# Kernel optimization log

Measured on AMD Instinct MI355X. Metric: run time of the kernel, lower is better.

Reference implementation:

```python
import jax, jax.numpy as jnp
import numpy as np

B = 16384   # batch
S = 512     # state_size
A = 512     # action_size
H = 1024    # hidden_dim
L = 64      # latent_size
E = 6       # num_experts
G = 32      # gate hidden size
IN = S + L      # first-layer input size
INT = H + L     # intermediate input size
SIGMA = 0.05


def setup_inputs() -> dict:
    key = jax.random.key(0)
    ks = jax.random.split(key, 20)

    def u(k, shape, s):
        return jax.random.uniform(k, shape, jnp.float32, -s, s)

    inp = {}
    inp['state'] = jax.random.normal(ks[0], (B, S), jnp.float32)
    inp['latent'] = jax.random.normal(ks[1], (B, L), jnp.float32)
    # expert decoder layers: (E, J, K) weights, (E, K) biases; torch init: w ~ U(-3/sqrt(J), 3/sqrt(J)), b ~ U(-1/sqrt(J), 1/sqrt(J))
    dims = [(IN, H), (INT, H), (INT, H), (INT, A)]
    for i, (j, k_) in enumerate(dims):
        stdv = 1.0 / np.sqrt(j)
        inp[f'w{i}'] = u(ks[2 + 2 * i], (E, j, k_), 3.0 * stdv)
        inp[f'b{i}'] = u(ks[3 + 2 * i], (E, k_), stdv)
    # gating MLP: IN -> G -> G -> E
    gdims = [(IN, G), (G, G), (G, E)]
    for i, (a, b) in enumerate(gdims):
        s = 1.0 / np.sqrt(a)
        inp[f'gw{i}'] = u(ks[10 + 2 * i], (a, b), s)
        inp[f'gb{i}'] = u(ks[11 + 2 * i], (b,), s)
    return inp


def reference(state, latent, w0, b0, w1, b1, w2, b2, w3, b3,
              gw0, gb0, gw1, gb1, gw2, gb2):
    xc = jnp.concatenate([state, latent], axis=-1)          # [B, IN]
    # gating MLP with ELU activations, softmax over experts
    h = jax.nn.elu(xc @ gw0 + gb0)
    h = jax.nn.elu(h @ gw1 + gb1)
    coef = jax.nn.softmax(h @ gw2 + gb2, axis=-1)           # [B, E]

    layer_out = state
    ws = [w0, w1, w2, w3]
    bs = [b0, b1, b2, b3]
    for i in range(4):
        inp = jnp.concatenate([layer_out, latent], axis=-1)  # [B, J]
        # per-sample soft-mixed expert matmul + bias
        mixed = jnp.einsum('be,bj,ejk->bk', coef, inp, ws[i],
                           optimize=True) + coef @ bs[i]      # [B, K]
        layer_out = jax.nn.elu(mixed) if i < 3 else mixed

    # reparameterize with fixed sigma: mu + eps * sigma (eps from a fixed key for determinism)
    eps = jax.random.normal(jax.random.key(42), layer_out.shape, layer_out.dtype)
    return layer_out + eps * SIGMA
```

## Files before the change

kernel.cpp:

```cpp
#include <hip/hip_runtime.h>

typedef _Float16 f16;
typedef _Float16 half8 __attribute__((ext_vector_type(8)));
typedef float f32x4 __attribute__((ext_vector_type(4)));
typedef unsigned int u32;

#define B_    16384
#define E_    6
#define ASTR  1088
#define AOUT  512

__device__ __forceinline__ u32 swz(u32 row, u32 ch) {
  return row * 128u + ((ch ^ (row & 7u)) * 16u);
}

__device__ __forceinline__ float elu_f(float x) {
  return x > 0.f ? x : (__expf(x) - 1.f);
}

__device__ __forceinline__ half8 splat8(f16 s) {
  half8 v = {s, s, s, s, s, s, s, s};
  return v;
}

__device__ __forceinline__ void gload16(const f16* g, char* l) {
  __builtin_amdgcn_global_load_lds(
      (const __attribute__((address_space(1))) void*)g,
      (__attribute__((address_space(3))) void*)l, 16, 0, 0);
}

#define WAITVM(N) asm volatile("s_waitcnt vmcnt(" #N ")" ::: "memory")

__device__ __forceinline__ float jax_eps(u32 idx) {
  const u32 k0 = 0u, k1 = 42u;
  const u32 k2 = k0 ^ k1 ^ 0x1BD11BDAu;
  u32 x0 = 0u + k0, x1 = idx + k1;
#define TFR(r) { x0 += x1; x1 = (x1 << (r)) | (x1 >> (32 - (r))); x1 ^= x0; }
  TFR(13) TFR(15) TFR(26) TFR(6)   x0 += k1; x1 += k2 + 1u;
  TFR(17) TFR(29) TFR(16) TFR(24)  x0 += k2; x1 += k0 + 2u;
  TFR(13) TFR(15) TFR(26) TFR(6)   x0 += k0; x1 += k1 + 3u;
  TFR(17) TFR(29) TFR(16) TFR(24)  x0 += k1; x1 += k2 + 4u;
  TFR(13) TFR(15) TFR(26) TFR(6)   x0 += k2; x1 += k0 + 5u;
#undef TFR
  u32 bits = x0 ^ x1;
  float f = __uint_as_float(0x3f800000u | (bits >> 9)) - 1.0f;
  const float lo = -0.99999994f;
  float u = fmaxf(lo, fmaf(f, 2.0f, lo));
  float w = -__logf(fmaf(-u, u, 1.0f));
  float p;
  if (w < 5.0f) {
    w -= 2.5f;
    p = 2.81022636e-08f;
    p = fmaf(p, w, 3.43273939e-07f);
    p = fmaf(p, w, -3.5233877e-06f);
    p = fmaf(p, w, -4.39150654e-06f);
    p = fmaf(p, w, 0.00021858087f);
    p = fmaf(p, w, -0.00125372503f);
    p = fmaf(p, w, -0.00417768164f);
    p = fmaf(p, w, 0.246640727f);
    p = fmaf(p, w, 1.50140941f);
  } else {
    w = __fsqrt_rn(w) - 3.0f;
    p = -0.000200214257f;
    p = fmaf(p, w, 0.000100950558f);
    p = fmaf(p, w, 0.00134934322f);
    p = fmaf(p, w, -0.00367342844f);
    p = fmaf(p, w, 0.00573950773f);
    p = fmaf(p, w, -0.0076224613f);
    p = fmaf(p, w, 0.00943887047f);
    p = fmaf(p, w, 1.00167406f);
    p = fmaf(p, w, 2.83297682f);
  }
  return 1.41421356f * p * u;
}

__global__ void prep_act(const float* __restrict__ state, const float* __restrict__ latent,
                         f16* __restrict__ actA, f16* __restrict__ actB) {
  const u32 NS = (B_ * 512u) / 8u;
  const u32 NL = (B_ * 64u) / 8u;
  u32 i = blockIdx.x * 256u + threadIdx.x;
  if (i < NS) {
    u32 e = i * 8u;
    u32 b = e >> 9, c = e & 511u;
    float4 v0 = *(const float4*)(state + e);
    float4 v1 = *(const float4*)(state + e + 4);
    half8 h;
    h[0]=(f16)v0.x; h[1]=(f16)v0.y; h[2]=(f16)v0.z; h[3]=(f16)v0.w;
    h[4]=(f16)v1.x; h[5]=(f16)v1.y; h[6]=(f16)v1.z; h[7]=(f16)v1.w;
    *(half8*)(actA + (size_t)b * ASTR + c) = h;
  } else if (i < NS + NL) {
    u32 e = (i - NS) * 8u;
    u32 b = e >> 6, c = e & 63u;
    float4 v0 = *(const float4*)(latent + e);
    float4 v1 = *(const float4*)(latent + e + 4);
    half8 h;
    h[0]=(f16)v0.x; h[1]=(f16)v0.y; h[2]=(f16)v0.z; h[3]=(f16)v0.w;
    h[4]=(f16)v1.x; h[5]=(f16)v1.y; h[6]=(f16)v1.z; h[7]=(f16)v1.w;
    *(half8*)(actA + (size_t)b * ASTR + 512 + c) = h;
    *(half8*)(actA + (size_t)b * ASTR + 1024 + c) = h;
    *(half8*)(actB + (size_t)b * ASTR + 1024 + c) = h;
  }
}

__global__ void prep_gw0(const float* __restrict__ gw0, f16* __restrict__ g0hi,
                         f16* __restrict__ g0lo) {
  int i = blockIdx.x * 256 + threadIdx.x;
  if (i < 32 * 576) {
    int n = i / 576, j = i % 576;
    float v = gw0[j * 32 + n];
    f16 h = (f16)v;
    g0hi[i] = h;
    g0lo[i] = (f16)(v - (float)h);
  }
}

__global__ void transpose_w(const float* __restrict__ w, f16* __restrict__ wt,
                            int J, int K) {
  __shared__ float t[64][65];
  int tiles_j = J >> 6, tiles_k = K >> 6;
  int per_e = tiles_j * tiles_k;
  int bid = blockIdx.x;
  int e = bid / per_e, rem = bid % per_e;
  int jt = rem / tiles_k, kt = rem % tiles_k;
  int tid = threadIdx.x;
  int r = tid >> 2, c0 = (tid & 3) << 4;
  const float* src = w + ((size_t)e * J + (size_t)jt * 64 + r) * K + (size_t)kt * 64 + c0;
  float4 v0 = *(const float4*)(src);
  float4 v1 = *(const float4*)(src + 4);
  float4 v2 = *(const float4*)(src + 8);
  float4 v3 = *(const float4*)(src + 12);
  t[r][c0+0]=v0.x;  t[r][c0+1]=v0.y;  t[r][c0+2]=v0.z;  t[r][c0+3]=v0.w;
  t[r][c0+4]=v1.x;  t[r][c0+5]=v1.y;  t[r][c0+6]=v1.z;  t[r][c0+7]=v1.w;
  t[r][c0+8]=v2.x;  t[r][c0+9]=v2.y;  t[r][c0+10]=v2.z; t[r][c0+11]=v2.w;
  t[r][c0+12]=v3.x; t[r][c0+13]=v3.y; t[r][c0+14]=v3.z; t[r][c0+15]=v3.w;
  __syncthreads();
  int kr = tid >> 2, jq = (tid & 3) << 4;
  half8 p0, p1;
#pragma unroll
  for (int m = 0; m < 8; m++) {
    p0[m] = (f16)t[jq + m][kr];
    p1[m] = (f16)t[jq + 8 + m][kr];
  }
  f16* dst = wt + ((size_t)e * K + (size_t)kt * 64 + kr) * J + (size_t)jt * 64 + jq;
  *(half8*)(dst) = p0;
  *(half8*)(dst + 8) = p1;
}

__global__ __launch_bounds__(256) void gating_kernel(
    const float* __restrict__ state, const float* __restrict__ latent,
    const f16* __restrict__ g0hi, const f16* __restrict__ g0lo,
    const float* __restrict__ gb0, const float* __restrict__ gw1,
    const float* __restrict__ gb1, const float* __restrict__ gw2,
    const float* __restrict__ gb2, float* __restrict__ coefT) {
  __shared__ __align__(16) char sm[24576];
  __shared__ float h_lds[64][33];
  char* Ahi = sm;
  char* Alo = sm + 8192;
  char* Bhi = sm + 16384;
  char* Blo = sm + 20480;
  const int tid = threadIdx.x, lane = tid & 63, wave = tid >> 6;
  const int b0 = blockIdx.x * 64;

  f32x4 acc[2];
#pragma unroll
  for (int n = 0; n < 2; n++) {
    float v = gb0[n * 16 + (lane & 15)];
    f32x4 t = {v, v, v, v};
    acc[n] = t;
  }

  for (int kt = 0; kt < 9; ++kt) {
    __syncthreads();
    int r = tid >> 2, cq = (tid & 3) << 4;
    float xv[16];
    if (kt < 8) {
      const float* s = state + (size_t)(b0 + r) * 512 + kt * 64 + cq;
      *(float4*)(xv)      = *(const float4*)(s);
      *(float4*)(xv + 4)  = *(const float4*)(s + 4);
      *(float4*)(xv + 8)  = *(const float4*)(s + 8);
      *(float4*)(xv + 12) = *(const float4*)(s + 12);
    } else {
      const float* s = latent + (size_t)(b0 + r) * 64 + cq;
      *(float4*)(xv)      = *(const float4*)(s);
      *(float4*)(xv + 4)  = *(const float4*)(s + 4);
      *(float4*)(xv + 8)  = *(const float4*)(s + 8);
      *(float4*)(xv + 12) = *(const float4*)(s + 12);
    }
    half8 hh[2], hl[2];
#pragma unroll
    for (int q = 0; q < 2; q++)
#pragma unroll
      for (int i = 0; i < 8; i++) {
        float x = xv[q * 8 + i];
        f16 h = (f16)x;
        hh[q][i] = h;
        hl[q][i] = (f16)(x - (float)h);
      }
    *(half8*)(Ahi + swz(r, (tid & 3) * 2 + 0)) = hh[0];
    *(half8*)(Ahi + swz(r, (tid & 3) * 2 + 1)) = hh[1];
    *(half8*)(Alo + swz(r, (tid & 3) * 2 + 0)) = hl[0];
    *(half8*)(Alo + swz(r, (tid & 3) * 2 + 1)) = hl[1];
    int nb = tid >> 3, chb = tid & 7;
    half8 bh = *(const half8*)(g0hi + (size_t)nb * 576 + kt * 64 + chb * 8);
    half8 bl = *(const half8*)(g0lo + (size_t)nb * 576 + kt * 64 + chb * 8);
    *(half8*)(Bhi + swz(nb, chb)) = bh;
    *(half8*)(Blo + swz(nb, chb)) = bl;
    __syncthreads();
#pragma unroll
    for (int ks = 0; ks < 2; ks++) {
      int arow = wave * 16 + (lane & 15);
      int ch = ks * 4 + (lane >> 4);
      half8 ah = *(const half8*)(Ahi + swz(arow, ch));
      half8 al = *(const half8*)(Alo + swz(arow, ch));
#pragma unroll
      for (int n = 0; n < 2; n++) {
        int brow = n * 16 + (lane & 15);
        half8 wh = *(const half8*)(Bhi + swz(brow, ch));
        half8 wl = *(const half8*)(Blo + swz(brow, ch));
        acc[n] = __builtin_amdgcn_mfma_f32_16x16x32_f16(ah, wh, acc[n], 0, 0, 0);
        acc[n] = __builtin_amdgcn_mfma_f32_16x16x32_f16(al, wh, acc[n], 0, 0, 0);
        acc[n] = __builtin_amdgcn_mfma_f32_16x16x32_f16(ah, wl, acc[n], 0, 0, 0);
      }
    }
  }
#pragma unroll
  for (int n = 0; n < 2; n++)
#pragma unroll
    for (int i = 0; i < 4; i++) {
      int row = wave * 16 + (lane >> 4) * 4 + i;
      int col = n * 16 + (lane & 15);
      h_lds[row][col] = elu_f(acc[n][i]);
    }
  __syncthreads();
  {
    int row = tid & 63, q = tid >> 6;
    float a2[8];
#pragma unroll
    for (int o = 0; o < 8; o++) a2[o] = gb1[q * 8 + o];
    for (int j = 0; j < 32; j++) {
      float v = h_lds[row][j];
#pragma unroll
      for (int o = 0; o < 8; o++) a2[o] = fmaf(v, gw1[j * 32 + q * 8 + o], a2[o]);
    }
    __syncthreads();
#pragma unroll
    for (int o = 0; o < 8; o++) h_lds[row][q * 8 + o] = elu_f(a2[o]);
  }
  __syncthreads();
  if (wave == 0) {
    float lg[6];
#pragma unroll
    for (int e = 0; e < 6; e++) lg[e] = gb2[e];
    for (int j = 0; j < 32; j++) {
      float v = h_lds[lane][j];
#pragma unroll
      for (int e = 0; e < 6; e++) lg[e] = fmaf(v, gw2[j * 6 + e], lg[e]);
    }
    float mx = lg[0];
#pragma unroll
    for (int e = 1; e < 6; e++) mx = fmaxf(mx, lg[e]);
    float s = 0.f, pc[6];
#pragma unroll
    for (int e = 0; e < 6; e++) { pc[e] = __expf(lg[e] - mx); s += pc[e]; }
    float inv = 1.0f / s;
#pragma unroll
    for (int e = 0; e < 6; e++) coefT[e * B_ + b0 + lane] = pc[e] * inv;
  }
}

template <int J, int KOUT, int MODE>
__global__ __launch_bounds__(256, 3) void moe_gemm(
    const f16* __restrict__ act, const f16* __restrict__ wt,
    const float* __restrict__ coefT, const float* __restrict__ bias,
    f16* __restrict__ out_act, float* __restrict__ out_f32) {
  constexpr int NSUB = J / 64;
  constexpr int NTILE = KOUT / 64;
  __shared__ __align__(16) char sm[44032];
  float* const cfLds = (float*)(sm + 40960);

  const int tid = threadIdx.x;
  const int lane = tid & 63;
  const int wv = tid >> 6;
  const int wr = wv >> 1, wc = wv & 1;
  const int nwg = gridDim.x;
  const int cpx = nwg >> 3;
  const int bid = (blockIdx.x & 7) * cpx + (blockIdx.x >> 3);
  const int b0 = (bid / NTILE) * 128;
  const int n0 = (bid % NTILE) * 64;

  for (int i = tid; i < E_ * 128; i += 256) {
    int e = i >> 7, r = i & 127;
    cfLds[i] = coefT[e * B_ + b0 + r];
  }
  __syncthreads();

  f32x4 acc[4][2];
#pragma unroll
  for (int m = 0; m < 4; m++)
#pragma unroll
    for (int n = 0; n < 2; n++) {
      f32x4 z = {0.f, 0.f, 0.f, 0.f};
      acc[m][n] = z;
    }
#pragma unroll
  for (int e = 0; e < E_; e++) {
    float bv[2];
#pragma unroll
    for (int n = 0; n < 2; n++)
      bv[n] = bias[e * KOUT + n0 + wc * 32 + n * 16 + (lane & 15)];
#pragma unroll
    for (int m = 0; m < 4; m++)
#pragma unroll
      for (int i = 0; i < 4; i++) {
        float cv = cfLds[e * 128 + wr * 64 + m * 16 + (lane >> 4) * 4 + i];
#pragma unroll
        for (int n = 0; n < 2; n++) acc[m][n][i] = fmaf(cv, bv[n], acc[m][n][i]);
      }
  }

  u32 aVoff[4], bVoff[2];
#pragma unroll
  for (int i = 0; i < 4; i++) {
    int r = wv * 32 + i * 8 + (lane >> 3);
    aVoff[i] = (u32)(b0 + r) * ASTR + (u32)(((lane & 7) ^ (r & 7)) * 8);
  }
#pragma unroll
  for (int i = 0; i < 2; i++) {
    int r = wv * 16 + i * 8 + (lane >> 3);
    bVoff[i] = (u32)(n0 + r) * J + (u32)(((lane & 7) ^ (r & 7)) * 8);
  }

  char* const As = sm;

  auto stageA = [&](int ks) {
    const f16* ab = act + ks * 64;
#pragma unroll
    for (int i = 0; i < 4; i++)
      gload16(ab + aVoff[i], As + (wv * 4 + i) * 1024);
  };
  auto stageB = [&](int e, int ks, int buf) {
    const f16* wb = wt + (size_t)e * KOUT * J + ks * 64;
    char* Bs = sm + 16384 + buf * 8192;
#pragma unroll
    for (int i = 0; i < 2; i++)
      gload16(wb + bVoff[i], Bs + (wv * 2 + i) * 1024);
  };

  stageA(0);
  stageB(0, 0, 0);
  stageB(1, 0, 1);

  u32 aOff[2], bOff[2];
#pragma unroll
  for (int h = 0; h < 2; h++) {
    aOff[h] = swz(wr * 64 + (lane & 15), h * 4 + (lane >> 4));
    bOff[h] = swz(wc * 32 + (lane & 15), h * 4 + (lane >> 4));
  }
  const u32 cfOff = (u32)(wr * 64 + (lane & 15)) * 4u;

  half8 afr[2][4];

  auto compute = [&](int buf, int e, bool loadA) {
    char* Bcur = sm + 16384 + buf * 8192;
    if (loadA) {
#pragma unroll
      for (int h = 0; h < 2; h++)
#pragma unroll
        for (int m = 0; m < 4; m++)
          afr[h][m] = *(const half8*)(As + aOff[h] + m * 2048);
    }
    f16 cfh[4];
#pragma unroll
    for (int m = 0; m < 4; m++)
      cfh[m] = (f16)*(const float*)((const char*)cfLds + cfOff + e * 512 + m * 64);
#pragma unroll
    for (int h = 0; h < 2; h++) {
      half8 bf[2];
#pragma unroll
      for (int n = 0; n < 2; n++)
        bf[n] = *(const half8*)(Bcur + bOff[h] + n * 2048);
      __builtin_amdgcn_s_setprio(1);
#pragma unroll
      for (int m = 0; m < 4; m++) {
        half8 afs = afr[h][m] * splat8(cfh[m]);
#pragma unroll
        for (int n = 0; n < 2; n++)
          acc[m][n] = __builtin_amdgcn_mfma_f32_16x16x32_f16(afs, bf[n], acc[m][n], 0, 0, 0);
      }
      __builtin_amdgcn_s_setprio(0);
    }
  };

  for (int ks = 0; ks < NSUB - 1; ++ks) {
#pragma unroll
    for (int e = 0; e < 6; ++e) {
      if (e == 2 || e == 3) { WAITVM(6); } else { WAITVM(2); }
      __builtin_amdgcn_s_barrier();
      stageB((e + 2) % 6, ks + (e + 2) / 6, (e + 2) % 3);
      if (e == 1) stageA(ks + 1);
      compute(e % 3, e, e == 0);
    }
  }
  {
    const int ks = NSUB - 1;
#pragma unroll
    for (int e = 0; e < 6; ++e) {
      if (e == 5) { WAITVM(0); } else { WAITVM(2); }
      __builtin_amdgcn_s_barrier();
      if (e <= 3) stageB(e + 2, ks, (e + 2) % 3);
      compute(e % 3, e, e == 0);
    }
  }

#pragma unroll
  for (int m = 0; m < 4; m++)
#pragma unroll
    for (int n = 0; n < 2; n++)
#pragma unroll
      for (int i = 0; i < 4; i++) {
        int row = b0 + wr * 64 + m * 16 + (lane >> 4) * 4 + i;
        int col = n0 + wc * 32 + n * 16 + (lane & 15);
        float x = acc[m][n][i];
        if (MODE == 0) {
          out_act[(size_t)row * ASTR + col] = (f16)elu_f(x);
        } else {
          u32 idx = (u32)row * AOUT + col;
          out_f32[idx] = fmaf(0.05f, jax_eps(idx), x);
        }
      }
}

extern "C" void kernel_launch(void* const* d_in, const int* in_sizes, int n_in,
                              void* d_out, int out_size, void* d_ws, size_t ws_size,
                              hipStream_t stream) {
  (void)in_sizes; (void)n_in; (void)out_size; (void)ws_size;
  const float* state  = (const float*)d_in[0];
  const float* latent = (const float*)d_in[1];
  const float* w0 = (const float*)d_in[2];
  const float* b0 = (const float*)d_in[3];
  const float* w1 = (const float*)d_in[4];
  const float* b1 = (const float*)d_in[5];
  const float* w2 = (const float*)d_in[6];
  const float* b2 = (const float*)d_in[7];
  const float* w3 = (const float*)d_in[8];
  const float* b3 = (const float*)d_in[9];
  const float* gw0 = (const float*)d_in[10];
  const float* gb0 = (const float*)d_in[11];
  const float* gw1 = (const float*)d_in[12];
  const float* gb1 = (const float*)d_in[13];
  const float* gw2 = (const float*)d_in[14];
  const float* gb2 = (const float*)d_in[15];

  char* ws = (char*)d_ws;
  size_t off = 0;
  float* coefT = (float*)(ws + off); off += (size_t)E_ * B_ * 4;
  f16* actA = (f16*)(ws + off); off += (size_t)B_ * ASTR * 2;
  f16* actB = (f16*)(ws + off); off += (size_t)B_ * ASTR * 2;
  f16* wt0 = (f16*)(ws + off); off += (size_t)E_ * 1024 * 576 * 2;
  f16* wt1 = (f16*)(ws + off); off += (size_t)E_ * 1024 * 1088 * 2;
  f16* wt2 = (f16*)(ws + off); off += (size_t)E_ * 1024 * 1088 * 2;
  f16* wt3 = (f16*)(ws + off); off += (size_t)E_ * 512 * 1088 * 2;
  f16* g0hi = (f16*)(ws + off); off += 32 * 576 * 2;
  f16* g0lo = (f16*)(ws + off); off += 32 * 576 * 2;

  prep_act<<<4608, 256, 0, stream>>>(state, latent, actA, actB);
  prep_gw0<<<72, 256, 0, stream>>>(gw0, g0hi, g0lo);
  transpose_w<<<6 * 9 * 16, 256, 0, stream>>>(w0, wt0, 576, 1024);
  transpose_w<<<6 * 17 * 16, 256, 0, stream>>>(w1, wt1, 1088, 1024);
  transpose_w<<<6 * 17 * 16, 256, 0, stream>>>(w2, wt2, 1088, 1024);
  transpose_w<<<6 * 17 * 8, 256, 0, stream>>>(w3, wt3, 1088, 512);
  gating_kernel<<<256, 256, 0, stream>>>(state, latent, g0hi, g0lo, gb0, gw1, gb1,
                                         gw2, gb2, coefT);
  moe_gemm<576, 1024, 0><<<2048, 256, 0, stream>>>(actA, wt0, coefT, b0, actB, nullptr);
  moe_gemm<1088, 1024, 0><<<2048, 256, 0, stream>>>(actB, wt1, coefT, b1, actA, nullptr);
  moe_gemm<1088, 1024, 0><<<2048, 256, 0, stream>>>(actA, wt2, coefT, b2, actB, nullptr);
  moe_gemm<1088, 512, 1><<<1024, 256, 0, stream>>>(actB, wt3, coefT, b3, nullptr, (float*)d_out);
}
```

Measured before the change: 747.8 us.

## Software-pipeline LDS B-fragment reads into registers ahead of MFMA in MoE GEMM

Restructures the expert loop so the B-tile fragments for the next expert are read from LDS into a second register set while MFMAs for the current expert run (ping-pong bfA/bfB). It also prefetches three B stages up front and rewrites the loop as explicitly unrolled steps with lgkmcnt waits. Launch bounds are lowered from 3 to 2 waves-per-EU to give the compiler room for the extra fragment registers. The intent is to hide LDS read latency behind matrix math, at the cost of register pressure, possible lower occupancy, and more complex hand-scheduled synchronization.

```diff
diff --git a/kernel.cpp b/kernel.cpp
--- a/kernel.cpp
+++ b/kernel.cpp
@@ -30,6 +30,7 @@
 }
 
 #define WAITVM(N) asm volatile("s_waitcnt vmcnt(" #N ")" ::: "memory")
+#define LGKM0    asm volatile("s_waitcnt lgkmcnt(0)" ::: "memory")
 
 __device__ __forceinline__ float jax_eps(u32 idx) {
   const u32 k0 = 0u, k1 = 42u;
@@ -269,7 +270,7 @@
 }
 
 template <int J, int KOUT, int MODE>
-__global__ __launch_bounds__(256, 3) void moe_gemm(
+__global__ __launch_bounds__(256, 2) void moe_gemm(
     const f16* __restrict__ act, const f16* __restrict__ wt,
     const float* __restrict__ coefT, const float* __restrict__ bias,
     f16* __restrict__ out_act, float* __restrict__ out_f32) {
@@ -277,6 +278,10 @@
   constexpr int NTILE = KOUT / 64;
   __shared__ __align__(16) char sm[44032];
   float* const cfLds = (float*)(sm + 40960);
+  char* const As  = sm;
+  char* const B0s = sm + 16384;
+  char* const B1s = sm + 24576;
+  char* const B2s = sm + 32768;
 
   const int tid = threadIdx.x;
   const int lane = tid & 63;
@@ -330,86 +335,129 @@
     bVoff[i] = (u32)(n0 + r) * J + (u32)(((lane & 7) ^ (r & 7)) * 8);
   }
 
-  char* const As = sm;
-
   auto stageA = [&](int ks) {
     const f16* ab = act + ks * 64;
 #pragma unroll
     for (int i = 0; i < 4; i++)
       gload16(ab + aVoff[i], As + (wv * 4 + i) * 1024);
   };
-  auto stageB = [&](int e, int ks, int buf) {
+  auto stageB = [&](int e, int ks, char* Bs) {
     const f16* wb = wt + (size_t)e * KOUT * J + ks * 64;
-    char* Bs = sm + 16384 + buf * 8192;
 #pragma unroll
     for (int i = 0; i < 2; i++)
       gload16(wb + bVoff[i], Bs + (wv * 2 + i) * 1024);
   };
 
   stageA(0);
-  stageB(0, 0, 0);
-  stageB(1, 0, 1);
-
-  u32 aOff[2], bOff[2];
+  stageB(0, 0, B0s);
+  stageB(1, 0, B1s);
+  stageB(2, 0, B2s);
+
+  u32 aOffh[2], bOffh[2];
 #pragma unroll
   for (int h = 0; h < 2; h++) {
-    aOff[h] = swz(wr * 64 + (lane & 15), h * 4 + (lane >> 4));
-    bOff[h] = swz(wc * 32 + (lane & 15), h * 4 + (lane >> 4));
+    aOffh[h] = swz(wr * 64 + (lane & 15), h * 4 + (lane >> 4));
+    bOffh[h] = swz(wc * 32 + (lane & 15), h * 4 + (lane >> 4));
   }
   const u32 cfOff = (u32)(wr * 64 + (lane & 15)) * 4u;
 
   half8 afr[2][4];
-
-  auto compute = [&](int buf, int e, bool loadA) {
-    char* Bcur = sm + 16384 + buf * 8192;
-    if (loadA) {
-#pragma unroll
-      for (int h = 0; h < 2; h++)
-#pragma unroll
-        for (int m = 0; m < 4; m++)
-          afr[h][m] = *(const half8*)(As + aOff[h] + m * 2048);
-    }
+  half8 bfA[2][2];
+  half8 bfB[2][2];
+
+  auto READA = [&]() {
+#pragma unroll
+    for (int h = 0; h < 2; h++)
+#pragma unroll
+      for (int m = 0; m < 4; m++)
+        afr[h][m] = *(const half8*)(As + aOffh[h] + m * 2048);
+  };
+  auto READB = [&](half8 (&bf)[2][2], const char* Bs) {
+#pragma unroll
+    for (int h = 0; h < 2; h++)
+#pragma unroll
+      for (int n = 0; n < 2; n++)
+        bf[h][n] = *(const half8*)(Bs + bOffh[h] + n * 2048);
+  };
+  auto DOMFMA = [&](const half8 (&bf)[2][2], int e) {
     f16 cfh[4];
 #pragma unroll
     for (int m = 0; m < 4; m++)
       cfh[m] = (f16)*(const float*)((const char*)cfLds + cfOff + e * 512 + m * 64);
 #pragma unroll
     for (int h = 0; h < 2; h++) {
-      half8 bf[2];
-#pragma unroll
-      for (int n = 0; n < 2; n++)
-        bf[n] = *(const half8*)(Bcur + bOff[h] + n * 2048);
       __builtin_amdgcn_s_setprio(1);
 #pragma unroll
       for (int m = 0; m < 4; m++) {
         half8 afs = afr[h][m] * splat8(cfh[m]);
 #pragma unroll
         for (int n = 0; n < 2; n++)
-          acc[m][n] = __builtin_amdgcn_mfma_f32_16x16x32_f16(afs, bf[n], acc[m][n], 0, 0, 0);
+          acc[m][n] = __builtin_amdgcn_mfma_f32_16x16x32_f16(afs, bf[h][n], acc[m][n], 0, 0, 0);
       }
       __builtin_amdgcn_s_setprio(0);
     }
   };
 
+  WAITVM(4);
+  __builtin_amdgcn_s_barrier();
+  READA();
+  READB(bfA, B0s);
+
   for (int ks = 0; ks < NSUB - 1; ++ks) {
-#pragma unroll
-    for (int e = 0; e < 6; ++e) {
-      if (e == 2 || e == 3) { WAITVM(6); } else { WAITVM(2); }
-      __builtin_amdgcn_s_barrier();
-      stageB((e + 2) % 6, ks + (e + 2) / 6, (e + 2) % 3);
-      if (e == 1) stageA(ks + 1);
-      compute(e % 3, e, e == 0);
-    }
+    WAITVM(2); __builtin_amdgcn_s_barrier(); LGKM0;
+    stageB(3, ks, B0s);
+    READB(bfB, B1s);
+    DOMFMA(bfA, 0);
+    WAITVM(2); __builtin_amdgcn_s_barrier(); LGKM0;
+    stageB(4, ks, B1s);
+    stageA(ks + 1);
+    READB(bfA, B2s);
+    DOMFMA(bfB, 1);
+    WAITVM(6); __builtin_amdgcn_s_barrier(); LGKM0;
+    stageB(5, ks, B2s);
+    READB(bfB, B0s);
+    DOMFMA(bfA, 2);
+    WAITVM(6); __builtin_amdgcn_s_barrier(); LGKM0;
+    stageB(0, ks + 1, B0s);
+    READB(bfA, B1s);
+    DOMFMA(bfB, 3);
+    WAITVM(2); __builtin_amdgcn_s_barrier(); LGKM0;
+    stageB(1, ks + 1, B1s);
+    READB(bfB, B2s);
+    DOMFMA(bfA, 4);
+    WAITVM(2); __builtin_amdgcn_s_barrier(); LGKM0;
+    stageB(2, ks + 1, B2s);
+    READB(bfA, B0s);
+    DOMFMA(bfB, 5);
+    READA();
   }
   {
-    const int ks = NSUB - 1;
-#pragma unroll
-    for (int e = 0; e < 6; ++e) {
-      if (e == 5) { WAITVM(0); } else { WAITVM(2); }
-      __builtin_amdgcn_s_barrier();
-      if (e <= 3) stageB(e + 2, ks, (e + 2) % 3);
-      compute(e % 3, e, e == 0);
-    }
+    const int F = NSUB - 1;
+    WAITVM(2); __builtin_amdgcn_s_barrier(); LGKM0;
+    stageB(3, F, B0s);
+    READB(bfB, B1s);
+    DOMFMA(bfA, 0);
+
+    WAITVM(2); __builtin_amdgcn_s_barrier(); LGKM0;
+    stageB(4, F, B1s);
+    READB(bfA, B2s);
+    DOMFMA(bfB, 1);
+
+    WAITVM(2); __builtin_amdgcn_s_barrier(); LGKM0;
+    stageB(5, F, B2s);
+    READB(bfB, B0s);
+    DOMFMA(bfA, 2);
+
+    WAITVM(2); __builtin_amdgcn_s_barrier(); LGKM0;
+    READB(bfA, B1s);
+    DOMFMA(bfB, 3);
+
+    WAITVM(0); __builtin_amdgcn_s_barrier(); LGKM0;
+    READB(bfB, B2s);
+    DOMFMA(bfA, 4);
+
+    __builtin_amdgcn_s_barrier();
+    DOMFMA(bfB, 5);
   }
 
 #pragma unroll
```

New measurement: 745.9 us. No clear change (-0.2%).

## Enlarge MoE GEMM tiles to 256xBN with 512-thread blocks and restructured pipeline

Applied to the files above, without the earlier changes.

Raises the moe_gemm block tile from 128x64 to 256x256 (256x128 for the last layer) using 8 waves per block, each holding a 128xBN/4 accumulator set. The explicitly unrolled per-expert staging schedule now prefetches B tiles into a 3-slot ring and loads A once per k-step. The goal is more reuse of A and B per LDS byte and fewer redundant global loads of weights. The cost is higher register pressure, more LDS per block, and only 256 blocks, which may leave some CUs underoccupied or unevenly loaded.

```diff
diff --git a/kernel.cpp b/kernel.cpp
--- a/kernel.cpp
+++ b/kernel.cpp
@@ -268,158 +268,210 @@
   }
 }
 
-template <int J, int KOUT, int MODE>
-__global__ __launch_bounds__(256, 3) void moe_gemm(
+template <int J, int KOUT, int BN, int MODE>
+__global__ __launch_bounds__(512) void moe_gemm(
     const f16* __restrict__ act, const f16* __restrict__ wt,
     const float* __restrict__ coefT, const float* __restrict__ bias,
     f16* __restrict__ out_act, float* __restrict__ out_f32) {
   constexpr int NSUB = J / 64;
-  constexpr int NTILE = KOUT / 64;
-  __shared__ __align__(16) char sm[44032];
-  float* const cfLds = (float*)(sm + 40960);
+  constexpr int NTILE = KOUT / BN;
+  constexpr int NF = BN / 64;
+  constexpr int BL = BN / 64;
+  constexpr u32 BSLOT = (u32)BN * 128u;
+  __shared__ __align__(16) char sm[32768 + 3 * BSLOT + 6144];
+  char* const As = sm;
+  float* const cfLds = (float*)(sm + 32768 + 3 * BSLOT);
 
   const int tid = threadIdx.x;
   const int lane = tid & 63;
   const int wv = tid >> 6;
-  const int wr = wv >> 1, wc = wv & 1;
+  const int wr = wv >> 2;
+  const int wc = wv & 3;
   const int nwg = gridDim.x;
   const int cpx = nwg >> 3;
   const int bid = (blockIdx.x & 7) * cpx + (blockIdx.x >> 3);
-  const int b0 = (bid / NTILE) * 128;
-  const int n0 = (bid % NTILE) * 64;
-
-  for (int i = tid; i < E_ * 128; i += 256) {
-    int e = i >> 7, r = i & 127;
+  const int b0 = (bid / NTILE) * 256;
+  const int n0 = (bid % NTILE) * BN;
+
+  for (int i = tid; i < E_ * 256; i += 512) {
+    int e = i >> 8, r = i & 255;
     cfLds[i] = coefT[e * B_ + b0 + r];
   }
   __syncthreads();
 
-  f32x4 acc[4][2];
-#pragma unroll
-  for (int m = 0; m < 4; m++)
-#pragma unroll
-    for (int n = 0; n < 2; n++) {
+  f32x4 acc[8][NF];
+#pragma unroll
+  for (int m = 0; m < 8; m++)
+#pragma unroll
+    for (int n = 0; n < NF; n++) {
       f32x4 z = {0.f, 0.f, 0.f, 0.f};
       acc[m][n] = z;
     }
 #pragma unroll
   for (int e = 0; e < E_; e++) {
-    float bv[2];
-#pragma unroll
-    for (int n = 0; n < 2; n++)
-      bv[n] = bias[e * KOUT + n0 + wc * 32 + n * 16 + (lane & 15)];
-#pragma unroll
-    for (int m = 0; m < 4; m++)
+    float bv[NF];
+#pragma unroll
+    for (int n = 0; n < NF; n++)
+      bv[n] = bias[e * KOUT + n0 + wc * (BN / 4) + n * 16 + (lane & 15)];
+#pragma unroll
+    for (int m = 0; m < 8; m++)
 #pragma unroll
       for (int i = 0; i < 4; i++) {
-        float cv = cfLds[e * 128 + wr * 64 + m * 16 + (lane >> 4) * 4 + i];
-#pragma unroll
-        for (int n = 0; n < 2; n++) acc[m][n][i] = fmaf(cv, bv[n], acc[m][n][i]);
+        float cv = cfLds[e * 256 + wr * 128 + m * 16 + (lane >> 4) * 4 + i];
+#pragma unroll
+        for (int n = 0; n < NF; n++) acc[m][n][i] = fmaf(cv, bv[n], acc[m][n][i]);
       }
   }
 
-  u32 aVoff[4], bVoff[2];
+  u32 aVoff[4], bVoff[BL];
 #pragma unroll
   for (int i = 0; i < 4; i++) {
-    int r = wv * 32 + i * 8 + (lane >> 3);
+    int r = i * 64 + wv * 8 + (lane >> 3);
     aVoff[i] = (u32)(b0 + r) * ASTR + (u32)(((lane & 7) ^ (r & 7)) * 8);
   }
 #pragma unroll
-  for (int i = 0; i < 2; i++) {
-    int r = wv * 16 + i * 8 + (lane >> 3);
+  for (int i = 0; i < BL; i++) {
+    int r = i * 64 + wv * 8 + (lane >> 3);
     bVoff[i] = (u32)(n0 + r) * J + (u32)(((lane & 7) ^ (r & 7)) * 8);
   }
-
-  char* const As = sm;
 
   auto stageA = [&](int ks) {
     const f16* ab = act + ks * 64;
 #pragma unroll
     for (int i = 0; i < 4; i++)
-      gload16(ab + aVoff[i], As + (wv * 4 + i) * 1024);
+      gload16(ab + aVoff[i], As + i * 8192 + wv * 1024);
   };
-  auto stageB = [&](int e, int ks, int buf) {
+  auto stageB = [&](int e, int ks, int slot) {
     const f16* wb = wt + (size_t)e * KOUT * J + ks * 64;
-    char* Bs = sm + 16384 + buf * 8192;
-#pragma unroll
-    for (int i = 0; i < 2; i++)
-      gload16(wb + bVoff[i], Bs + (wv * 2 + i) * 1024);
+    char* Bs = sm + 32768 + slot * BSLOT;
+#pragma unroll
+    for (int i = 0; i < BL; i++)
+      gload16(wb + bVoff[i], Bs + i * 8192 + wv * 1024);
   };
+
+  WAITVM(0);
 
   stageA(0);
   stageB(0, 0, 0);
   stageB(1, 0, 1);
 
-  u32 aOff[2], bOff[2];
+  u32 aOffh[2], bOffh[2];
 #pragma unroll
   for (int h = 0; h < 2; h++) {
-    aOff[h] = swz(wr * 64 + (lane & 15), h * 4 + (lane >> 4));
-    bOff[h] = swz(wc * 32 + (lane & 15), h * 4 + (lane >> 4));
-  }
-  const u32 cfOff = (u32)(wr * 64 + (lane & 15)) * 4u;
-
-  half8 afr[2][4];
-
-  auto compute = [&](int buf, int e, bool loadA) {
-    char* Bcur = sm + 16384 + buf * 8192;
-    if (loadA) {
-#pragma unroll
-      for (int h = 0; h < 2; h++)
-#pragma unroll
-        for (int m = 0; m < 4; m++)
-          afr[h][m] = *(const half8*)(As + aOff[h] + m * 2048);
-    }
-    f16 cfh[4];
-#pragma unroll
-    for (int m = 0; m < 4; m++)
-      cfh[m] = (f16)*(const float*)((const char*)cfLds + cfOff + e * 512 + m * 64);
-#pragma unroll
-    for (int h = 0; h < 2; h++) {
-      half8 bf[2];
-#pragma unroll
-      for (int n = 0; n < 2; n++)
-        bf[n] = *(const half8*)(Bcur + bOff[h] + n * 2048);
-      __builtin_amdgcn_s_setprio(1);
-#pragma unroll
-      for (int m = 0; m < 4; m++) {
+    aOffh[h] = swz(wr * 128 + (lane & 15), h * 4 + (lane >> 4));
+    bOffh[h] = swz(wc * (BN / 4) + (lane & 15), h * 4 + (lane >> 4));
+  }
+  const u32 cfBase = (u32)(wr * 128 + (lane & 15)) * 4u;
+
+  half8 afr[2][8];
+  half8 bf[2][NF];
+
+  auto READA = [&]() {
+#pragma unroll
+    for (int h = 0; h < 2; h++)
+#pragma unroll
+      for (int m = 0; m < 8; m++)
+        afr[h][m] = *(const half8*)(As + aOffh[h] + m * 2048);
+  };
+  auto READB = [&](int slot) {
+    const char* Bs = sm + 32768 + slot * BSLOT;
+#pragma unroll
+    for (int h = 0; h < 2; h++)
+#pragma unroll
+      for (int n = 0; n < NF; n++)
+        bf[h][n] = *(const half8*)(Bs + bOffh[h] + n * 2048);
+  };
+  auto DOMFMA = [&](int e) {
+    f16 cfh[8];
+#pragma unroll
+    for (int m = 0; m < 8; m++)
+      cfh[m] = (f16)*(const float*)((const char*)cfLds + cfBase + e * 1024 + m * 64);
+    __builtin_amdgcn_s_setprio(1);
+#pragma unroll
+    for (int h = 0; h < 2; h++)
+#pragma unroll
+      for (int m = 0; m < 8; m++) {
         half8 afs = afr[h][m] * splat8(cfh[m]);
 #pragma unroll
-        for (int n = 0; n < 2; n++)
-          acc[m][n] = __builtin_amdgcn_mfma_f32_16x16x32_f16(afs, bf[n], acc[m][n], 0, 0, 0);
+        for (int n = 0; n < NF; n++)
+          acc[m][n] = __builtin_amdgcn_mfma_f32_16x16x32_f16(afs, bf[h][n], acc[m][n], 0, 0, 0);
       }
-      __builtin_amdgcn_s_setprio(0);
-    }
+    __builtin_amdgcn_s_setprio(0);
   };
 
+#define WAIT_BL()  do { if constexpr (BN == 256) { WAITVM(4); } else { WAITVM(2); } } while (0)
+#define WAIT_ABL() do { if constexpr (BN == 256) { WAITVM(8); } else { WAITVM(6); } } while (0)
+
   for (int ks = 0; ks < NSUB - 1; ++ks) {
-#pragma unroll
-    for (int e = 0; e < 6; ++e) {
-      if (e == 2 || e == 3) { WAITVM(6); } else { WAITVM(2); }
-      __builtin_amdgcn_s_barrier();
-      stageB((e + 2) % 6, ks + (e + 2) / 6, (e + 2) % 3);
-      if (e == 1) stageA(ks + 1);
-      compute(e % 3, e, e == 0);
-    }
+    WAIT_BL(); __builtin_amdgcn_s_barrier();
+    stageB(2, ks, 2);
+    READA();
+    READB(0);
+    DOMFMA(0);
+    WAIT_BL(); __builtin_amdgcn_s_barrier();
+    stageB(3, ks, 0);
+    stageA(ks + 1);
+    READB(1);
+    DOMFMA(1);
+    WAIT_ABL(); __builtin_amdgcn_s_barrier();
+    stageB(4, ks, 1);
+    READB(2);
+    DOMFMA(2);
+    WAIT_ABL(); __builtin_amdgcn_s_barrier();
+    stageB(5, ks, 2);
+    READB(0);
+    DOMFMA(3);
+    WAIT_BL(); __builtin_amdgcn_s_barrier();
+    stageB(0, ks + 1, 0);
+    READB(1);
+    DOMFMA(4);
+    WAIT_BL(); __builtin_amdgcn_s_barrier();
+    stageB(1, ks + 1, 1);
+    READB(2);
+    DOMFMA(5);
   }
   {
-    const int ks = NSUB - 1;
-#pragma unroll
-    for (int e = 0; e < 6; ++e) {
-      if (e == 5) { WAITVM(0); } else { WAITVM(2); }
-      __builtin_amdgcn_s_barrier();
-      if (e <= 3) stageB(e + 2, ks, (e + 2) % 3);
-      compute(e % 3, e, e == 0);
-    }
-  }
-
-#pragma unroll
-  for (int m = 0; m < 4; m++)
-#pragma unroll
-    for (int n = 0; n < 2; n++)
+    const int F = NSUB - 1;
+    WAIT_BL(); __builtin_amdgcn_s_barrier();
+    stageB(2, F, 2);
+    READA();
+    READB(0);
+    DOMFMA(0);
+
+    WAIT_BL(); __builtin_amdgcn_s_barrier();
+    stageB(3, F, 0);
+    READB(1);
+    DOMFMA(1);
+
+    WAIT_BL(); __builtin_amdgcn_s_barrier();
+    stageB(4, F, 1);
+    READB(2);
+    DOMFMA(2);
+
+    WAIT_BL(); __builtin_amdgcn_s_barrier();
+    stageB(5, F, 2);
+    READB(0);
+    DOMFMA(3);
+
+    WAIT_BL(); __builtin_amdgcn_s_barrier();
+    READB(1);
+    DOMFMA(4);
+
+    WAITVM(0); __builtin_amdgcn_s_barrier();
+    READB(2);
+    DOMFMA(5);
+  }
+#undef WAIT_BL
+#undef WAIT_ABL
+
+#pragma unroll
+  for (int m = 0; m < 8; m++)
+#pragma unroll
+    for (int n = 0; n < NF; n++)
 #pragma unroll
       for (int i = 0; i < 4; i++) {
-        int row = b0 + wr * 64 + m * 16 + (lane >> 4) * 4 + i;
-        int col = n0 + wc * 32 + n * 16 + (lane & 15);
+        int row = b0 + wr * 128 + m * 16 + (lane >> 4) * 4 + i;
+        int col = n0 + wc * (BN / 4) + n * 16 + (lane & 15);
         float x = acc[m][n][i];
         if (MODE == 0) {
           out_act[(size_t)row * ASTR + col] = (f16)elu_f(x);
@@ -471,8 +523,8 @@
   transpose_w<<<6 * 17 * 8, 256, 0, stream>>>(w3, wt3, 1088, 512);
   gating_kernel<<<256, 256, 0, stream>>>(state, latent, g0hi, g0lo, gb0, gw1, gb1,
                                          gw2, gb2, coefT);
-  moe_gemm<576, 1024, 0><<<2048, 256, 0, stream>>>(actA, wt0, coefT, b0, actB, nullptr);
-  moe_gemm<1088, 1024, 0><<<2048, 256, 0, stream>>>(actB, wt1, coefT, b1, actA, nullptr);
-  moe_gemm<1088, 1024, 0><<<2048, 256, 0, stream>>>(actA, wt2, coefT, b2, actB, nullptr);
-  moe_gemm<1088, 512, 1><<<1024, 256, 0, stream>>>(actB, wt3, coefT, b3, nullptr, (float*)d_out);
-}
+  moe_gemm<576, 1024, 256, 0><<<256, 512, 0, stream>>>(actA, wt0, coefT, b0, actB, nullptr);
+  moe_gemm<1088, 1024, 256, 0><<<256, 512, 0, stream>>>(actB, wt1, coefT, b1, actA, nullptr);
+  moe_gemm<1088, 1024, 256, 0><<<256, 512, 0, stream>>>(actA, wt2, coefT, b2, actB, nullptr);
+  moe_gemm<1088, 512, 128, 1><<<256, 512, 0, stream>>>(actB, wt3, coefT, b3, nullptr, (float*)d_out);
+}
```

Result: slower. 1.129 ms (+51.0%).
